# Optimization experiments

Measured on AMD Instinct MI355X. Metric: run time of the kernel, lower is better.

## Reference

```python
import jax, jax.numpy as jnp
import numpy as np

N_HEAD = 16
LN_EPS = 1e-5     # torch LayerNorm default
ATTN_EPS = 1e-6   # fast-transformers CausalLinearAttention eps


def layer_norm(x, g, b):
    mu = x.mean(-1, keepdims=True)
    var = ((x - mu) ** 2).mean(-1, keepdims=True)
    return (x - mu) * jax.lax.rsqrt(var + LN_EPS) * g + b


def favor(x, omega):
    # Favor/Performer softmax-kernel features.
    # x: [B,S,H,dh], omega: [dh, m/2] -> phi: [B,S,H,m] with m = 2*(dh//2) = dh
    dh = x.shape[-1]
    m = 2 * omega.shape[-1]
    xs = x * (dh ** -0.25)  # x * sqrt(softmax_temp), softmax_temp = 1/sqrt(dh)
    u = jnp.einsum('bshd,dm->bshm', xs, omega)
    h = 0.5 * jnp.sum(xs * xs, axis=-1, keepdims=True)  # ||x||^2 / 2
    return jnp.concatenate([jnp.exp(u - h), jnp.exp(-u - h)], axis=-1) * (m ** -0.5)


def causal_linear_attention(q, k, v):
    # q,k: [B,S,H,M] feature-mapped; v: [B,S,H,Dv]
    # out[i] = (phiQ_i @ sum_{j<=i} phiK_j v_j^T) / (phiQ_i . sum_{j<=i} phiK_j)
    B, S, H, M = q.shape
    Dv = v.shape[-1]
    qT = jnp.moveaxis(q, 1, 0)  # [S,B,H,M]
    kT = jnp.moveaxis(k, 1, 0)
    vT = jnp.moveaxis(v, 1, 0)  # [S,B,H,Dv]
    S0 = jnp.zeros((B, H, M, Dv), q.dtype)
    z0 = jnp.zeros((B, H, M), q.dtype)

    def step(carry, qkv):
        Sst, zst = carry
        qi, ki, vi = qkv
        Sst = Sst + ki[..., :, None] * vi[..., None, :]  # [B,H,M,Dv]
        zst = zst + ki                                   # [B,H,M]
        num = jnp.einsum('bhm,bhmd->bhd', qi, Sst)
        den = jnp.einsum('bhm,bhm->bh', qi, zst) + ATTN_EPS
        return (Sst, zst), num / den[..., None]

    _, out = jax.lax.scan(step, (S0, z0), (qT, kT, vT))
    return jnp.moveaxis(out, 0, 1)  # [B,S,H,Dv]


def forward(x, Wq, bq, Wk, bk, Wv, bv, Wo, bo, omega,
            ln1_g, ln1_b, ln2_g, ln2_b, W1, bf1, W2, bf2):
    L = Wq.shape[0]
    B, S, D = x.shape
    dh = D // N_HEAD
    out = x
    for l in range(L):  # fixed small layer count
        q = (out @ Wq[l] + bq[l]).reshape(B, S, N_HEAD, dh)
        k = (out @ Wk[l] + bk[l]).reshape(B, S, N_HEAD, dh)
        v = (out @ Wv[l] + bv[l]).reshape(B, S, N_HEAD, dh)
        Qf = favor(q, omega[l])
        Kf = favor(k, omega[l])
        a = causal_linear_attention(Qf, Kf, v).reshape(B, S, D)
        a = a @ Wo[l] + bo[l]
        h = layer_norm(out + a, ln1_g[l], ln1_b[l])          # norm1 (post-norm)
        y = jax.nn.relu(h @ W1[l] + bf1[l]) @ W2[l] + bf2[l]  # FFN
        out = layer_norm(h + y, ln2_g[l], ln2_b[l])          # norm2
    return out


def setup_inputs() -> dict:
    key = jax.random.key(0)
    L, B, S, D, DFF = 3, 2, 1024, 1024, 4096
    dh = D // N_HEAD
    ks = jax.random.split(key, 8)
    g = lambda k, shape: jax.random.normal(k, shape, jnp.float32) * 0.02
    return {
        'x': jax.random.normal(ks[0], (B, S, D), jnp.float32),
        'Wq': g(ks[1], (L, D, D)), 'bq': jnp.zeros((L, D), jnp.float32),
        'Wk': g(ks[2], (L, D, D)), 'bk': jnp.zeros((L, D), jnp.float32),
        'Wv': g(ks[3], (L, D, D)), 'bv': jnp.zeros((L, D), jnp.float32),
        'Wo': g(ks[4], (L, D, D)), 'bo': jnp.zeros((L, D), jnp.float32),
        'omega': jax.random.normal(ks[5], (L, dh, dh // 2), jnp.float32),
        'ln1_g': jnp.ones((L, D), jnp.float32), 'ln1_b': jnp.zeros((L, D), jnp.float32),
        'ln2_g': jnp.ones((L, D), jnp.float32), 'ln2_b': jnp.zeros((L, D), jnp.float32),
        'W1': g(ks[6], (L, D, DFF)), 'bf1': jnp.zeros((L, DFF), jnp.float32),
        'W2': g(ks[7], (L, DFF, D)), 'bf2': jnp.zeros((L, D), jnp.float32),
    }


def reference(x, Wq, bq, Wk, bk, Wv, bv, Wo, bo, omega,
              ln1_g, ln1_b, ln2_g, ln2_b, W1, bf1, W2, bf2):
    return forward(x, Wq, bq, Wk, bk, Wv, bv, Wo, bo, omega,
                   ln1_g, ln1_b, ln2_g, ln2_b, W1, bf1, W2, bf2)
```

## Files before the change

### kernel.cpp

```cpp
#include <hip/hip_runtime.h>

typedef unsigned int u32;
typedef unsigned short u16;
typedef unsigned long long u64;

#define LN_EPS 1e-5f
#define ATTN_EPS 1e-6f

typedef __bf16 bf16x8 __attribute__((ext_vector_type(8)));
typedef short shortx8 __attribute__((ext_vector_type(8)));
typedef float fx4 __attribute__((ext_vector_type(4)));
typedef float fx16 __attribute__((ext_vector_type(16)));

__device__ __forceinline__ u16 f2bf(float f){
  union{float f; u32 u;} x; x.f = f;
  u32 r = 0x7fffu + ((x.u>>16)&1u);
  return (u16)((x.u + r)>>16);
}
__device__ __forceinline__ float bf2f(u16 u){
  union{u32 u; float f;} x; x.u = ((u32)u)<<16; return x.f;
}
__device__ __forceinline__ bf16x8 ldfrag(const u16* p){
  return __builtin_bit_cast(bf16x8, *(const shortx8*)p);
}

__device__ __forceinline__ void async16(const void* g, void* l){
  typedef const __attribute__((address_space(1))) void gas_t;
  typedef __attribute__((address_space(3))) void las_t;
  __builtin_amdgcn_global_load_lds((gas_t*)(u64)g, (las_t*)(u32)(u64)l, 16, 0, 0);
}

__global__ void detect_kernel(const u16* __restrict__ ln1g, int* __restrict__ flag){
  if (threadIdx.x == 0 && blockIdx.x == 0)
    *flag = (ln1g[0] == 0x3F80u) ? 1 : 0;
}

__global__ __launch_bounds__(256) void cvt_small(
    const void* p0, const void* p1, const void* p2, const void* p3,
    const void* p4, const void* p5, const void* p6, const void* p7,
    const void* p8, const void* p9, const void* p10,
    float* __restrict__ out, const int* __restrict__ flagp)
{
  int i = blockIdx.x*256 + threadIdx.x;
  if (i >= 46080) return;
  const void* src; int off;
  if      (i < 3072)  { src=p0;  off=i; }
  else if (i < 6144)  { src=p1;  off=i-3072; }
  else if (i < 9216)  { src=p2;  off=i-6144; }
  else if (i < 12288) { src=p3;  off=i-9216; }
  else if (i < 18432) { src=p4;  off=i-12288; }
  else if (i < 21504) { src=p5;  off=i-18432; }
  else if (i < 24576) { src=p6;  off=i-21504; }
  else if (i < 27648) { src=p7;  off=i-24576; }
  else if (i < 30720) { src=p8;  off=i-27648; }
  else if (i < 43008) { src=p9;  off=i-30720; }
  else                { src=p10; off=i-43008; }
  float v;
  if (*flagp){ union{u32 u; float f;} x; x.u = ((u32)((const u16*)src)[off])<<16; v = x.f; }
  else v = ((const float*)src)[off];
  out[i] = v;
}

__global__ __launch_bounds__(256) void cvt_x(const void* __restrict__ in, float* __restrict__ out,
                                             u16* __restrict__ outbf, int n, const int* __restrict__ flagp){
  int i = blockIdx.x*256 + threadIdx.x;
  if (i >= n) return;
  float v;
  if (*flagp){ union{u32 u; float f;} x; x.u = ((u32)((const u16*)in)[i])<<16; v = x.f; }
  else v = ((const float*)in)[i];
  out[i] = v;
  outbf[i] = f2bf(v);
}

__global__ __launch_bounds__(256) void transpose_cvtL(
    const void* __restrict__ W, u16* __restrict__ Wt,
    int K, int N, size_t zsrc, size_t zdst, const int* __restrict__ flagp)
{
  __shared__ float s[32][33];
  const size_t eoff = (size_t)blockIdx.z * zsrc;
  Wt += (size_t)blockIdx.z * zdst;
  const int bx = blockIdx.x, by = blockIdx.y;
  const int tid = threadIdx.x;
  const int c = tid & 31, r = tid >> 5;
  const int isbf = *flagp;
#pragma unroll
  for (int i = 0; i < 4; ++i){
    int k = by*32 + r + i*8, n = bx*32 + c;
    size_t idx = eoff + (size_t)k*N + n;
    float v;
    if (isbf){ union{u32 u; float f;} x; x.u = ((u32)((const u16*)W)[idx])<<16; v = x.f; }
    else v = ((const float*)W)[idx];
    s[r + i*8][c] = v;
  }
  __syncthreads();
#pragma unroll
  for (int i = 0; i < 4; ++i){
    int n = bx*32 + r + i*8, k = by*32 + c;
    Wt[(size_t)n*K + k] = f2bf(s[c][r + i*8]);
  }
}

__global__ __launch_bounds__(256) void transpose_cvtQ(
    const void* __restrict__ W0, const void* __restrict__ W1,
    const void* __restrict__ W2, const void* __restrict__ W3,
    u16* __restrict__ Wt, const int* __restrict__ flagp)
{
  __shared__ float s[32][33];
  const int z = blockIdx.z, l = z >> 2, m = z & 3;
  const void* W = (m==0)?W0:((m==1)?W1:((m==2)?W2:W3));
  const size_t eoff = (size_t)l * 1048576;
  Wt += (size_t)z * 1048576;
  const int bx = blockIdx.x, by = blockIdx.y;
  const int tid = threadIdx.x;
  const int c = tid & 31, r = tid >> 5;
  const int isbf = *flagp;
#pragma unroll
  for (int i = 0; i < 4; ++i){
    int k = by*32 + r + i*8, n = bx*32 + c;
    size_t idx = eoff + (size_t)k*1024 + n;
    float v;
    if (isbf){ union{u32 u; float f;} x; x.u = ((u32)((const u16*)W)[idx])<<16; v = x.f; }
    else v = ((const float*)W)[idx];
    s[r + i*8][c] = v;
  }
  __syncthreads();
#pragma unroll
  for (int i = 0; i < 4; ++i){
    int n = bx*32 + r + i*8, k = by*32 + c;
    Wt[(size_t)n*1024 + k] = f2bf(s[c][r + i*8]);
  }
}

__global__ __launch_bounds__(256, 2) void mfma_gemm(
    const u16* __restrict__ A, const u16* __restrict__ W,
    const float* __restrict__ bias,
    float* __restrict__ C, u16* __restrict__ Cbf,
    int N, int Kst, int kstep_z, int klen,
    size_t wz, size_t cz, int bz, int bias_all, int relu)
{
  __shared__ u16 As[3][128*32];
  __shared__ u16 Bs[3][128*32];
  const int z = blockIdx.z;
  W    += (size_t)z * wz;
  bias += (size_t)z * bz;
  if (C) C += (size_t)z * cz;
  const int kbeg = z * kstep_z;
  const int tid = threadIdx.x;
  const int lane = tid & 63, wid = tid >> 6;

  int bx = blockIdx.x, by = blockIdx.y;
  {
    const int gx = gridDim.x, gy = gridDim.y;
    if (((gx & 3) == 0 || gx == 2 || gx == 8) && ((gy & 1) == 0)) {
    }
    if (((gx & 3) == 0) && ((gy & 1) == 0)) {
      const int cw = gx >> 2, ch = gy >> 1;
      if (((cw & (cw-1)) == 0) && ((ch & (ch-1)) == 0)) {
        const int o = by*gx + bx;
        const int xcd = o & 7, k = o >> 3;
        const int lgw = 31 - __clz(cw);
        bx = (xcd & 3)*cw + (k & (cw-1));
        by = (xcd >> 2)*ch + (k >> lgw);
      }
    }
  }
  const int row0 = by * 128, col0 = bx * 128;

  const int sR = 32*wid + (lane >> 2);
  const int sC = (((lane & 3) ^ ((lane >> 2) & 3))) << 3;
  const u16* gA  = A + (size_t)(row0 + sR)*Kst + kbeg + sC;
  const u16* gAj = gA + (size_t)16 * Kst;
  const u16* gB  = W + (size_t)(col0 + sR)*Kst + kbeg + sC;
  const u16* gBj = gB + (size_t)16 * Kst;
  const int lb = wid*1024 + lane*8;

  const int iters = klen >> 5;
#pragma unroll
  for (int s = 0; s < 2; ++s){
    const int ko = s*32;
    async16(gA  + ko, &As[s][lb]);
    async16(gAj + ko, &As[s][lb + 512]);
    async16(gB  + ko, &Bs[s][lb]);
    async16(gBj + ko, &Bs[s][lb + 512]);
  }

  const int l31 = lane & 31, hi = lane >> 5;
  const int wr = (wid >> 1) * 64, wc = (wid & 1) * 64;
  const int rc0 = ((hi     ^ (lane & 3))) << 3;
  const int rc1 = (((2+hi) ^ (lane & 3))) << 3;
  fx16 acc[2][2] = {};

  for (int it = 0; it < iters; ++it){
    const int cur = it % 3;
    __builtin_amdgcn_s_waitcnt(0x0F74);
    __builtin_amdgcn_s_barrier();
    {
      const int nx   = (it + 2 < iters) ? (it + 2) : (iters - 1);
      const int nbuf = (it + 2) % 3;
      const int ko = nx*32;
      async16(gA  + ko, &As[nbuf][lb]);
      async16(gAj + ko, &As[nbuf][lb + 512]);
      async16(gB  + ko, &Bs[nbuf][lb]);
      async16(gBj + ko, &Bs[nbuf][lb + 512]);
    }
    bf16x8 a0k0 = ldfrag(&As[cur][(wr      + l31)*32 + rc0]);
    bf16x8 a1k0 = ldfrag(&As[cur][(wr + 32 + l31)*32 + rc0]);
    bf16x8 b0k0 = ldfrag(&Bs[cur][(wc      + l31)*32 + rc0]);
    bf16x8 b1k0 = ldfrag(&Bs[cur][(wc + 32 + l31)*32 + rc0]);
    bf16x8 a0k1 = ldfrag(&As[cur][(wr      + l31)*32 + rc1]);
    bf16x8 a1k1 = ldfrag(&As[cur][(wr + 32 + l31)*32 + rc1]);
    bf16x8 b0k1 = ldfrag(&Bs[cur][(wc      + l31)*32 + rc1]);
    bf16x8 b1k1 = ldfrag(&Bs[cur][(wc + 32 + l31)*32 + rc1]);
    acc[0][0] = __builtin_amdgcn_mfma_f32_32x32x16_bf16(a0k0, b0k0, acc[0][0], 0,0,0);
    acc[0][1] = __builtin_amdgcn_mfma_f32_32x32x16_bf16(a0k0, b1k0, acc[0][1], 0,0,0);
    acc[1][0] = __builtin_amdgcn_mfma_f32_32x32x16_bf16(a1k0, b0k0, acc[1][0], 0,0,0);
    acc[1][1] = __builtin_amdgcn_mfma_f32_32x32x16_bf16(a1k0, b1k0, acc[1][1], 0,0,0);
    acc[0][0] = __builtin_amdgcn_mfma_f32_32x32x16_bf16(a0k1, b0k1, acc[0][0], 0,0,0);
    acc[0][1] = __builtin_amdgcn_mfma_f32_32x32x16_bf16(a0k1, b1k1, acc[0][1], 0,0,0);
    acc[1][0] = __builtin_amdgcn_mfma_f32_32x32x16_bf16(a1k1, b0k1, acc[1][0], 0,0,0);
    acc[1][1] = __builtin_amdgcn_mfma_f32_32x32x16_bf16(a1k1, b1k1, acc[1][1], 0,0,0);
  }
  __builtin_amdgcn_s_waitcnt(0x0F70);

  const int rbase = 4*hi;
#pragma unroll
  for (int nt = 0; nt < 2; ++nt){
    const int col = col0 + wc + nt*32 + l31;
    const float bv = (bias_all || z == 0) ? bias[col] : 0.f;
#pragma unroll
    for (int mt = 0; mt < 2; ++mt){
#pragma unroll
      for (int r = 0; r < 16; ++r){
        const int row = row0 + wr + mt*32 + rbase + (r & 3) + 8*(r >> 2);
        float v = acc[mt][nt][r] + bv;
        if (relu) v = fmaxf(v, 0.f);
        if (C)   C[(size_t)row*N + col] = v;
        if (Cbf) Cbf[(size_t)row*N + col] = f2bf(v);
      }
    }
  }
}

__global__ __launch_bounds__(256) void favor_kernel(
    float* __restrict__ Q, float* __restrict__ Kp, const float* __restrict__ omega,
    u16* __restrict__ Qb, u16* __restrict__ Kb)
{
  __shared__ float sh[4][64];
  __shared__ float sho[64][32];
  int tid = threadIdx.x;
  for (int i = tid; i < 2048; i += 256)
    sho[i>>5][i&31] = omega[i];
  int wv = tid >> 6, lane = tid & 63;
  int th = blockIdx.x*4 + wv;
  size_t base = (size_t)(th >> 4) * 1024 + (size_t)(th & 15) * 64;
  int jm = lane & 31;
  float sgn = (lane < 32) ? 1.f : -1.f;
  for (int w = 0; w < 2; ++w){
    float* p = w ? Kp : Q;
    float xs = p[base + lane] * 0.35355339059327373f;
    __syncthreads();
    sh[wv][lane] = xs;
    __syncthreads();
    float u = 0.f, hh = 0.f;
#pragma unroll
    for (int d = 0; d < 64; ++d){
      float xv = sh[wv][d];
      u  = fmaf(xv, sho[d][jm], u);
      hh = fmaf(xv, xv, hh);
    }
    float phi = expf(sgn*u - 0.5f*hh) * 0.125f;
    if (w) p[base + lane] = phi;
    (w ? Kb : Qb)[base + lane] = f2bf(phi);
  }
}

__global__ __launch_bounds__(256) void chunk_kv(
    const float* __restrict__ Kf, const float* __restrict__ V,
    float* __restrict__ KV, float* __restrict__ Ksum)
{
  __shared__ float Ks[64][64];
  __shared__ float Vs[64][64];
  int blk = blockIdx.x;
  int c = blk & 15, h = (blk >> 4) & 15, b = blk >> 8;
  int tid = threadIdx.x;
  for (int i = tid; i < 1024; i += 256){
    int j = i >> 4, m4 = (i & 15) << 2;
    size_t src = ((size_t)(b*1024 + c*64 + j)*16 + h)*64 + m4;
    *(float4*)&Ks[j][m4] = *(const float4*)&Kf[src];
    *(float4*)&Vs[j][m4] = *(const float4*)&V[src];
  }
  __syncthreads();
  int m = tid & 63, dg = tid >> 6;
  float acc[16] = {0.f};
  for (int j = 0; j < 64; ++j){
    float kv = Ks[j][m];
#pragma unroll
    for (int di = 0; di < 16; ++di)
      acc[di] = fmaf(Vs[j][dg*16+di], kv, acc[di]);
  }
  size_t outb = (size_t)blk * 4096;
#pragma unroll
  for (int di = 0; di < 16; ++di)
    KV[outb + (size_t)(dg*16+di)*64 + m] = acc[di];
  if (tid < 64){
    float s = 0.f;
    for (int j = 0; j < 64; ++j) s += Ks[j][tid];
    Ksum[(size_t)blk*64 + tid] = s;
  }
}

__global__ __launch_bounds__(256) void chunk_scan(float* __restrict__ KV, float* __restrict__ Ksum)
{
  int blk = blockIdx.x;
  int bh = blk >> 4, ec = blk & 15;
  int e = ec*256 + threadIdx.x;
  size_t base = (size_t)bh * 65536 + e;
  float run = 0.f;
  for (int c = 0; c < 16; ++c){
    size_t idx = base + (size_t)c*4096;
    float t = KV[idx]; KV[idx] = run; run += t;
  }
  if (ec == 0 && threadIdx.x < 64){
    size_t kb = (size_t)bh * 1024 + threadIdx.x;
    float rz = 0.f;
    for (int c = 0; c < 16; ++c){
      size_t idx = kb + c*64;
      float t = Ksum[idx]; Ksum[idx] = rz; rz += t;
    }
  }
}

__global__ __launch_bounds__(256) void attn_kernel(
    const u16* __restrict__ Qbf, const u16* __restrict__ Kbf,
    const float* __restrict__ V, const float* __restrict__ KVt,
    const float* __restrict__ Ksum, u16* __restrict__ Outbf)
{
  __shared__ u16 Qs[64][72];
  __shared__ u16 Ks[64][72];
  __shared__ u16 Ss[64][72];
  __shared__ u16 Vt[64][72];
  __shared__ u16 Pt[64][72];
  __shared__ float Vrow[64][68];
  __shared__ float densum[64];

  const int blk = blockIdx.x;
  const int c = blk & 15, h = (blk >> 4) & 15, b = blk >> 8;
  const int tid = threadIdx.x;
  const int lane = tid & 63, w = tid >> 6;
  const int quad = lane >> 4, l16 = lane & 15;
  const int t0 = b*1024 + c*64;

  {
    const int r = tid >> 2, q4 = (tid & 3) << 4;
    size_t g = (size_t)(t0 + r)*1024 + h*64 + q4;
    *(uint4*)&Qs[r][q4]   = *(const uint4*)(Qbf + g);
    *(uint4*)&Qs[r][q4+8] = *(const uint4*)(Qbf + g + 8);
    *(uint4*)&Ks[r][q4]   = *(const uint4*)(Kbf + g);
    *(uint4*)&Ks[r][q4+8] = *(const uint4*)(Kbf + g + 8);
    const float* vg = V + g;
    *(float4*)&Vrow[r][q4+0]  = *(const float4*)(vg+0);
    *(float4*)&Vrow[r][q4+4]  = *(const float4*)(vg+4);
    *(float4*)&Vrow[r][q4+8]  = *(const float4*)(vg+8);
    *(float4*)&Vrow[r][q4+12] = *(const float4*)(vg+12);
    const float* pg = KVt + (size_t)blk*4096 + r*64 + q4;
    u16 tmp[16];
#pragma unroll
    for (int j = 0; j < 16; ++j) tmp[j] = f2bf(pg[j]);
    *(uint4*)&Pt[r][q4]   = *(uint4*)&tmp[0];
    *(uint4*)&Pt[r][q4+8] = *(uint4*)&tmp[8];
  }
  __syncthreads();
  {
    const int d = tid >> 2, j16 = (tid & 3) << 4;
    u16 tmp[16];
#pragma unroll
    for (int j = 0; j < 16; ++j) tmp[j] = f2bf(Vrow[j16+j][d]);
    *(uint4*)&Vt[d][j16]   = *(uint4*)&tmp[0];
    *(uint4*)&Vt[d][j16+8] = *(uint4*)&tmp[8];
  }

  const int iw0 = w*16;
  bf16x8 aq0 = ldfrag(&Qs[iw0+l16][quad*8]);
  bf16x8 aq1 = ldfrag(&Qs[iw0+l16][32+quad*8]);
  fx4 sacc[4];
#pragma unroll
  for (int u = 0; u < 4; ++u){
    sacc[u] = (fx4){0.f,0.f,0.f,0.f};
    bf16x8 b0 = ldfrag(&Ks[u*16+l16][quad*8]);
    bf16x8 b1 = ldfrag(&Ks[u*16+l16][32+quad*8]);
    sacc[u] = __builtin_amdgcn_mfma_f32_16x16x32_bf16(aq0, b0, sacc[u], 0, 0, 0);
    sacc[u] = __builtin_amdgcn_mfma_f32_16x16x32_bf16(aq1, b1, sacc[u], 0, 0, 0);
  }
  float rs[4] = {0.f,0.f,0.f,0.f};
#pragma unroll
  for (int u = 0; u < 4; ++u){
    const int jl = u*16 + l16;
#pragma unroll
    for (int r = 0; r < 4; ++r){
      const int il = iw0 + quad*4 + r;
      float v = (jl <= il) ? sacc[u][r] : 0.f;
      rs[r] += v;
      Ss[il][jl] = f2bf(v);
    }
  }
#pragma unroll
  for (int off = 1; off < 16; off <<= 1){
#pragma unroll
    for (int r = 0; r < 4; ++r) rs[r] += __shfl_xor(rs[r], off);
  }
  if (l16 == 0){
#pragma unroll
    for (int r = 0; r < 4; ++r) densum[iw0 + quad*4 + r] = rs[r];
  }
  __syncthreads();

  {
    const int row = iw0 + l16;
    const float* zp = Ksum + (size_t)blk*64;
    float dp = 0.f;
#pragma unroll
    for (int m = 0; m < 16; ++m){
      const int mm = quad*16 + m;
      dp = fmaf(bf2f(Qs[row][mm]), zp[mm], dp);
    }
    dp += __shfl_xor(dp, 16);
    dp += __shfl_xor(dp, 32);
    if (quad == 0) densum[row] = densum[row] + dp + ATTN_EPS;
  }
  __syncthreads();

  bf16x8 as0 = ldfrag(&Ss[iw0+l16][quad*8]);
  bf16x8 as1 = ldfrag(&Ss[iw0+l16][32+quad*8]);
  fx4 oacc[4];
#pragma unroll
  for (int u = 0; u < 4; ++u){
    const int d0 = u*16;
    oacc[u] = (fx4){0.f,0.f,0.f,0.f};
    oacc[u] = __builtin_amdgcn_mfma_f32_16x16x32_bf16(as0, ldfrag(&Vt[d0+l16][quad*8]),    oacc[u], 0,0,0);
    oacc[u] = __builtin_amdgcn_mfma_f32_16x16x32_bf16(as1, ldfrag(&Vt[d0+l16][32+quad*8]), oacc[u], 0,0,0);
    oacc[u] = __builtin_amdgcn_mfma_f32_16x16x32_bf16(aq0, ldfrag(&Pt[d0+l16][quad*8]),    oacc[u], 0,0,0);
    oacc[u] = __builtin_amdgcn_mfma_f32_16x16x32_bf16(aq1, ldfrag(&Pt[d0+l16][32+quad*8]), oacc[u], 0,0,0);
  }
#pragma unroll
  for (int u = 0; u < 4; ++u){
    const int d = u*16 + l16;
#pragma unroll
    for (int r = 0; r < 4; ++r){
      const int il = iw0 + quad*4 + r;
      const float o = oacc[u][r] / densum[il];
      Outbf[(size_t)(t0 + il)*1024 + h*64 + d] = f2bf(o);
    }
  }
}

__global__ __launch_bounds__(256) void resid_ln(
    const float* __restrict__ X, const float* __restrict__ Y0, const float* __restrict__ Y1,
    const float* __restrict__ Y2, const float* __restrict__ Y3,
    const float* __restrict__ g, const float* __restrict__ b,
    float* __restrict__ Dst, u16* __restrict__ DstBf,
    void* __restrict__ OutPtr, const int* __restrict__ flagp)
{
  __shared__ float rs[4], rss[4];
  int row = blockIdx.x, tid = threadIdx.x;
  int lane = tid & 63, wv = tid >> 6;
  size_t base = (size_t)row * 1024;
  int c = tid << 2;
  float4 xv = *(const float4*)&X[base + c];
  float4 y0 = *(const float4*)&Y0[base + c];
  float4 y1 = *(const float4*)&Y1[base + c];
  float v0 = xv.x+y0.x+y1.x, v1 = xv.y+y0.y+y1.y, v2 = xv.z+y0.z+y1.z, v3 = xv.w+y0.w+y1.w;
  if (Y2){
    float4 y2 = *(const float4*)&Y2[base + c];
    float4 y3 = *(const float4*)&Y3[base + c];
    v0 += y2.x + y3.x; v1 += y2.y + y3.y; v2 += y2.z + y3.z; v3 += y2.w + y3.w;
  }
  float s = v0+v1+v2+v3;
  float ss = v0*v0+v1*v1+v2*v2+v3*v3;
  for (int off = 32; off; off >>= 1){
    s  += __shfl_down(s, off);
    ss += __shfl_down(ss, off);
  }
  if (lane == 0){ rs[wv] = s; rss[wv] = ss; }
  __syncthreads();
  float S  = rs[0]+rs[1]+rs[2]+rs[3];
  float SS = rss[0]+rss[1]+rss[2]+rss[3];
  float mu = S * (1.f/1024.f);
  float var = SS * (1.f/1024.f) - mu*mu;
  float rinv = rsqrtf(var + LN_EPS);
  float4 gv = *(const float4*)(g + c);
  float4 bb = *(const float4*)(b + c);
  float o0 = (v0-mu)*rinv*gv.x + bb.x;
  float o1 = (v1-mu)*rinv*gv.y + bb.y;
  float o2 = (v2-mu)*rinv*gv.z + bb.z;
  float o3 = (v3-mu)*rinv*gv.w + bb.w;
  *(float4*)&Dst[base + c] = make_float4(o0,o1,o2,o3);
  uint2 ob;
  ob.x = (u32)f2bf(o0) | ((u32)f2bf(o1) << 16);
  ob.y = (u32)f2bf(o2) | ((u32)f2bf(o3) << 16);
  *(uint2*)(DstBf + base + c) = ob;
  if (OutPtr){
    if (*flagp){
      *(uint2*)((u16*)OutPtr + base + c) = ob;
    } else {
      *(float4*)((float*)OutPtr + base + c) = make_float4(o0,o1,o2,o3);
    }
  }
}

extern "C" void kernel_launch(void* const* d_in, const int* in_sizes, int n_in,
                              void* d_out, int out_size, void* d_ws, size_t ws_size,
                              hipStream_t stream)
{
  (void)in_sizes; (void)n_in; (void)out_size; (void)ws_size;

  float* ws   = (float*)d_ws;
  float* R    = ws;
  float* P0   = R  + 2097152;
  float* P1   = P0 + 2097152;
  float* P2   = P1 + 2097152;
  float* P3   = P2 + 2097152;
  float* KVb  = P3 + 2097152;
  float* Ks   = KVb + 2097152;
  float* smallP = Ks + 32768;
  float* pend = smallP + 46080;
  int* flag = (int*)pend;
  u16* abf  = (u16*)(pend + 4);
  u16* hbf  = abf  + 2097152;
  u16* t1bf = hbf  + 2097152;
  u16* fbf  = t1bf + 2097152;
  u16* qpbf = fbf  + 8388608;
  u16* kpbf = qpbf + 2097152;
  u16* WtQ  = kpbf + 2097152;
  u16* WtF1 = WtQ  + 12582912;
  u16* WtF2 = WtF1 + 12582912;

  float* bqF  = smallP + 0;
  float* boF  = smallP + 9216;
  float* omF  = smallP + 12288;
  float* l1gF = smallP + 18432;
  float* l1bF = smallP + 21504;
  float* l2gF = smallP + 24576;
  float* l2bF = smallP + 27648;
  float* bf1F = smallP + 30720;
  float* bf2F = smallP + 43008;

  detect_kernel<<<1, 64, 0, stream>>>((const u16*)d_in[10], flag);
  cvt_small<<<180, 256, 0, stream>>>(d_in[2], d_in[4], d_in[6], d_in[8], d_in[9],
                                     d_in[10], d_in[11], d_in[12], d_in[13],
                                     d_in[15], d_in[17], smallP, flag);
  cvt_x<<<8192, 256, 0, stream>>>(d_in[0], R, abf, 2097152, flag);

  transpose_cvtQ<<<dim3(32, 32, 12), 256, 0, stream>>>(d_in[1], d_in[3], d_in[5], d_in[7],
                                                       WtQ, flag);
  transpose_cvtL<<<dim3(128, 32, 3), 256, 0, stream>>>(d_in[14], WtF1, 1024, 4096,
                                                       4194304, 4194304, flag);
  transpose_cvtL<<<dim3(32, 128, 3), 256, 0, stream>>>(d_in[16], WtF2, 4096, 1024,
                                                       4194304, 4194304, flag);

  dim3 gQKV(8, 16, 3);
  dim3 gO(8, 16, 2);
  dim3 gF1(32, 16, 1);
  dim3 gF2(8, 16, 4);

  for (int l = 0; l < 3; ++l){
    const size_t wQ = (size_t)l * 4194304;

    mfma_gemm<<<gQKV, 256, 0, stream>>>(abf, WtQ + wQ, bqF + l*1024, P0, (u16*)nullptr,
                                        1024, 1024, 0, 1024,
                                        1048576, 2097152, 3072, 1, 0);
    favor_kernel<<<8192, 256, 0, stream>>>(P0, P1, omF + l*2048, qpbf, kpbf);
    chunk_kv<<<512, 256, 0, stream>>>(P1, P2, KVb, Ks);
    chunk_scan<<<512, 256, 0, stream>>>(KVb, Ks);
    attn_kernel<<<512, 256, 0, stream>>>(qpbf, kpbf, P2, KVb, Ks, t1bf);

    mfma_gemm<<<gO, 256, 0, stream>>>(t1bf, WtQ + wQ + 3145728, boF + l*1024, P0, (u16*)nullptr,
                                      1024, 1024, 512, 512,
                                      0, 2097152, 0, 0, 0);
    resid_ln<<<2048, 256, 0, stream>>>(R, P0, P1, nullptr, nullptr,
                                       l1gF + l*1024, l1bF + l*1024,
                                       KVb, hbf, nullptr, flag);

    mfma_gemm<<<gF1, 256, 0, stream>>>(hbf, WtF1 + wQ, bf1F + l*4096, (float*)nullptr, fbf,
                                       4096, 1024, 0, 1024,
                                       0, 0, 0, 1, 1);

    mfma_gemm<<<gF2, 256, 0, stream>>>(fbf, WtF2 + wQ, bf2F + l*1024, P0, (u16*)nullptr,
                                       1024, 4096, 1024, 1024,
                                       0, 2097152, 0, 0, 0);

    resid_ln<<<2048, 256, 0, stream>>>(KVb, P0, P1, P2, P3,
                                       l2gF + l*1024, l2bF + l*1024,
                                       R, abf, (l == 2) ? d_out : nullptr, flag);
  }
}
```

Baseline: 786.2 us.

## Switch GEMM main loop to double-buffered BK=64 tiles with 8-way swizzle

Replaces the 3-stage BK=32 shared-memory pipeline in the MFMA GEMM with a 2-stage BK=64 pipeline. Each thread now loads a row segment with an 8-wide XOR swizzle, all fragments for four k-substeps are loaded before eight MFMAs per tile pair, and s_setprio raises priority around the MFMA block. The aim is fewer barriers and waits per unit of K work, and more MFMA work between synchronisations. In exchange there is one fewer prefetch stage of latency hiding and more registers held for the preloaded fragments.

```diff
diff --git a/kernel.cpp b/kernel.cpp
--- a/kernel.cpp
+++ b/kernel.cpp
@@ -138,8 +138,8 @@
     int N, int Kst, int kstep_z, int klen,
     size_t wz, size_t cz, int bz, int bias_all, int relu)
 {
-  __shared__ u16 As[3][128*32];
-  __shared__ u16 Bs[3][128*32];
+  __shared__ u16 As[2][128*64];
+  __shared__ u16 Bs[2][128*64];
   const int z = blockIdx.z;
   W    += (size_t)z * wz;
   bias += (size_t)z * bz;
@@ -151,8 +151,6 @@
   int bx = blockIdx.x, by = blockIdx.y;
   {
     const int gx = gridDim.x, gy = gridDim.y;
-    if (((gx & 3) == 0 || gx == 2 || gx == 8) && ((gy & 1) == 0)) {
-    }
     if (((gx & 3) == 0) && ((gy & 1) == 0)) {
       const int cw = gx >> 2, ch = gy >> 1;
       if (((cw & (cw-1)) == 0) && ((ch & (ch-1)) == 0)) {
@@ -166,61 +164,56 @@
   }
   const int row0 = by * 128, col0 = bx * 128;
 
-  const int sR = 32*wid + (lane >> 2);
-  const int sC = (((lane & 3) ^ ((lane >> 2) & 3))) << 3;
-  const u16* gA  = A + (size_t)(row0 + sR)*Kst + kbeg + sC;
-  const u16* gAj = gA + (size_t)16 * Kst;
-  const u16* gB  = W + (size_t)(col0 + sR)*Kst + kbeg + sC;
-  const u16* gBj = gB + (size_t)16 * Kst;
-  const int lb = wid*1024 + lane*8;
-
-  const int iters = klen >> 5;
-#pragma unroll
-  for (int s = 0; s < 2; ++s){
-    const int ko = s*32;
-    async16(gA  + ko, &As[s][lb]);
-    async16(gAj + ko, &As[s][lb + 512]);
-    async16(gB  + ko, &Bs[s][lb]);
-    async16(gBj + ko, &Bs[s][lb + 512]);
-  }
+  const int sR = tid >> 3;
+  const int sC = ((tid & 7) ^ (sR & 7)) << 3;
+  const u16* gA = A + (size_t)(row0 + sR)*Kst + kbeg + sC;
+  const u16* gB = W + (size_t)(col0 + sR)*Kst + kbeg + sC;
+  const int lb = tid*8;
+
+  const int iters = klen >> 6;
+#pragma unroll
+  for (int i = 0; i < 4; ++i){
+    async16(gA + (size_t)(32*i)*Kst, &As[0][i*2048 + lb]);
+    async16(gB + (size_t)(32*i)*Kst, &Bs[0][i*2048 + lb]);
+  }
+  __builtin_amdgcn_s_waitcnt(0x0F70);
+  __builtin_amdgcn_s_barrier();
 
   const int l31 = lane & 31, hi = lane >> 5;
   const int wr = (wid >> 1) * 64, wc = (wid & 1) * 64;
-  const int rc0 = ((hi     ^ (lane & 3))) << 3;
-  const int rc1 = (((2+hi) ^ (lane & 3))) << 3;
   fx16 acc[2][2] = {};
 
-  for (int it = 0; it < iters; ++it){
-    const int cur = it % 3;
-    __builtin_amdgcn_s_waitcnt(0x0F74);
+  for (int t = 0; t < iters; ++t){
+    const int cur = t & 1;
+    if (t + 1 < iters){
+      const int ko = (t + 1) << 6;
+#pragma unroll
+      for (int i = 0; i < 4; ++i){
+        async16(gA + (size_t)(32*i)*Kst + ko, &As[cur^1][i*2048 + lb]);
+        async16(gB + (size_t)(32*i)*Kst + ko, &Bs[cur^1][i*2048 + lb]);
+      }
+    }
+    bf16x8 af0[4], af1[4], bg0[4], bg1[4];
+#pragma unroll
+    for (int kh = 0; kh < 4; ++kh){
+      const int sl = (((2*kh + hi) ^ (l31 & 7))) << 3;
+      af0[kh] = ldfrag(&As[cur][(wr      + l31)*64 + sl]);
+      af1[kh] = ldfrag(&As[cur][(wr + 32 + l31)*64 + sl]);
+      bg0[kh] = ldfrag(&Bs[cur][(wc      + l31)*64 + sl]);
+      bg1[kh] = ldfrag(&Bs[cur][(wc + 32 + l31)*64 + sl]);
+    }
+    __builtin_amdgcn_s_setprio(1);
+#pragma unroll
+    for (int kh = 0; kh < 4; ++kh){
+      acc[0][0] = __builtin_amdgcn_mfma_f32_32x32x16_bf16(af0[kh], bg0[kh], acc[0][0], 0,0,0);
+      acc[0][1] = __builtin_amdgcn_mfma_f32_32x32x16_bf16(af0[kh], bg1[kh], acc[0][1], 0,0,0);
+      acc[1][0] = __builtin_amdgcn_mfma_f32_32x32x16_bf16(af1[kh], bg0[kh], acc[1][0], 0,0,0);
+      acc[1][1] = __builtin_amdgcn_mfma_f32_32x32x16_bf16(af1[kh], bg1[kh], acc[1][1], 0,0,0);
+    }
+    __builtin_amdgcn_s_setprio(0);
+    __builtin_amdgcn_s_waitcnt(0x0F70);
     __builtin_amdgcn_s_barrier();
-    {
-      const int nx   = (it + 2 < iters) ? (it + 2) : (iters - 1);
-      const int nbuf = (it + 2) % 3;
-      const int ko = nx*32;
-      async16(gA  + ko, &As[nbuf][lb]);
-      async16(gAj + ko, &As[nbuf][lb + 512]);
-      async16(gB  + ko, &Bs[nbuf][lb]);
-      async16(gBj + ko, &Bs[nbuf][lb + 512]);
-    }
-    bf16x8 a0k0 = ldfrag(&As[cur][(wr      + l31)*32 + rc0]);
-    bf16x8 a1k0 = ldfrag(&As[cur][(wr + 32 + l31)*32 + rc0]);
-    bf16x8 b0k0 = ldfrag(&Bs[cur][(wc      + l31)*32 + rc0]);
-    bf16x8 b1k0 = ldfrag(&Bs[cur][(wc + 32 + l31)*32 + rc0]);
-    bf16x8 a0k1 = ldfrag(&As[cur][(wr      + l31)*32 + rc1]);
-    bf16x8 a1k1 = ldfrag(&As[cur][(wr + 32 + l31)*32 + rc1]);
-    bf16x8 b0k1 = ldfrag(&Bs[cur][(wc      + l31)*32 + rc1]);
-    bf16x8 b1k1 = ldfrag(&Bs[cur][(wc + 32 + l31)*32 + rc1]);
-    acc[0][0] = __builtin_amdgcn_mfma_f32_32x32x16_bf16(a0k0, b0k0, acc[0][0], 0,0,0);
-    acc[0][1] = __builtin_amdgcn_mfma_f32_32x32x16_bf16(a0k0, b1k0, acc[0][1], 0,0,0);
-    acc[1][0] = __builtin_amdgcn_mfma_f32_32x32x16_bf16(a1k0, b0k0, acc[1][0], 0,0,0);
-    acc[1][1] = __builtin_amdgcn_mfma_f32_32x32x16_bf16(a1k0, b1k0, acc[1][1], 0,0,0);
-    acc[0][0] = __builtin_amdgcn_mfma_f32_32x32x16_bf16(a0k1, b0k1, acc[0][0], 0,0,0);
-    acc[0][1] = __builtin_amdgcn_mfma_f32_32x32x16_bf16(a0k1, b1k1, acc[0][1], 0,0,0);
-    acc[1][0] = __builtin_amdgcn_mfma_f32_32x32x16_bf16(a1k1, b0k1, acc[1][0], 0,0,0);
-    acc[1][1] = __builtin_amdgcn_mfma_f32_32x32x16_bf16(a1k1, b1k1, acc[1][1], 0,0,0);
-  }
-  __builtin_amdgcn_s_waitcnt(0x0F70);
+  }
 
   const int rbase = 4*hi;
 #pragma unroll
```

New measurement: 727.5 us. 7.5% less time.
